# Performance work log

Measured on AMD Instinct MI355X. Metric: run time of the kernel, lower is better.

## Reference

```python
import jax, jax.numpy as jnp
import numpy as np

N, H, DDE, NH = 256, 256, 64, 4

def setup_inputs() -> dict:
    key = jax.random.key(0)
    ks = jax.random.split(key, 12)
    rn = lambda k, s, sc=1.0: (jax.random.normal(k, s) * sc).astype(jnp.float32)
    return {
        "action_hidden_state": rn(ks[0], (N, H)),
        "goal_hidden_state": rn(ks[1], (N, H)),
        "goal": rn(ks[2], (N, 2)),
        "action": rn(ks[3], (N, 2)),
        "W_dist": rn(ks[4], (8, DDE), 0.3),          # distEmbedding Linear(8, dde)
        "b_dist": jnp.zeros((DDE,), jnp.float32),
        "W_gate": rn(ks[5], (DDE, H), 0.1),          # gateFC Linear(dde, H)
        "b_gate": jnp.zeros((H,), jnp.float32),
        "w": rn(ks[6], (NH, 1, H, H), 0.06),         # GAT per-head projection
        "a": rn(ks[7], (1, 1, 2 * H, 1), 0.06),      # attention vector
        "bias": jnp.zeros((H,), jnp.float32),
    }

def reference(action_hidden_state, goal_hidden_state, goal, action,
              W_dist, b_dist, W_gate, b_gate, w, a, bias):
    n = goal.shape[0]
    # --- InteractionGate.cal_gate: x1[i,j] = x[j], x2[i,j] = x[i] ---
    g1 = jnp.broadcast_to(goal[None, :, :], (n, n, 2))
    g2 = jnp.broadcast_to(goal[:, None, :], (n, n, 2))
    a1 = jnp.broadcast_to(action[None, :, :], (n, n, 2))
    a2 = jnp.broadcast_to(action[:, None, :], (n, n, 2))
    dist = jnp.concatenate([a2, g2, a1, g1], axis=-1)                 # [n,n,8]
    gate = jax.nn.sigmoid(jax.nn.relu(dist @ W_dist + b_dist) @ W_gate + b_gate)  # [n,n,H]
    # temp_action_1[i,j] = action_hidden_state[j]
    gate_action = gate * jnp.tanh(action_hidden_state[None, :, :])    # [n,n,H]
    # diagonal entries replaced by goal_hidden_state (mask_goal = eye)
    eye = jnp.eye(n, dtype=bool)[:, :, None]
    gated_h = jnp.where(eye, goal_hidden_state[None, :, :], gate_action)  # [n,n,H]

    # --- GAT assembly: h_self[i,k] = ahs[i]; h_other = cat(ahs, gated_h) ---
    h_other = jnp.concatenate([action_hidden_state[:, None, :], gated_h], axis=1)  # [n,n+1,H]

    wm = w[:, 0]          # [NH,H,H]
    a_flat = a[0, 0, :, 0]  # [2H]
    f = wm.shape[-1]
    n_head = wm.shape[0]
    # h_self rows along k are all identical -> project once per (head, node)
    hsp = jnp.einsum('nh,zhf->znf', action_hidden_state, wm)          # [NH,n,f]
    hop = jnp.einsum('nkh,zhf->znkf', h_other, wm)                    # [NH,n,n+1,f]
    # cat([h_self', h_other']) @ a  ==  h_self'@a[:f] + h_other'@a[f:]
    score = (hsp @ a_flat[:f])[:, :, None] + hop @ a_flat[f:]         # [NH,n,n+1]
    e = jnp.where(score > 0, score, 0.2 * score)                      # LeakyReLU(0.2)
    alpha = jax.nn.softmax(e, axis=-1)                                # softmax over neighbors
    # h_attn = matmul(h_other, w) == hop; weighted sum over k, mean over heads
    out = jnp.einsum('znk,znkf->nf', alpha, hop) / n_head             # [n,f]
    return jax.nn.relu(out) + bias
```

## Files before the change

### kernel.cpp

```cpp
#include <hip/hip_runtime.h>
#include <hip/hip_bf16.h>

#define NN 256
#define HH 256

typedef __attribute__((ext_vector_type(8))) short short8;
typedef __attribute__((ext_vector_type(4))) short s16x4;
typedef __attribute__((ext_vector_type(4))) float f32x4;

__device__ __forceinline__ ushort f2bf(float x) {
    __hip_bfloat16 h = __float2bfloat16(x);
    return *reinterpret_cast<ushort*>(&h);
}
template <int CTRL>
__device__ __forceinline__ float dpp_add(float x) {
    int y = __builtin_amdgcn_update_dpp(0, __float_as_int(x), CTRL, 0xF, 0xF, true);
    return x + __int_as_float(y);
}
__device__ __forceinline__ float red16(float v) {
    v = dpp_add<0xB1>(v);
    v = dpp_add<0x4E>(v);
    v = dpp_add<0x141>(v);
    v = dpp_add<0x140>(v);
    return v;
}

#define WS_P   0
#define WS_Q   16384
#define WS_T   32768
#define WS_WA  98304
#define WS_WB  99328
#define WS_WGT 100352
#define WS_PV  104448
#define WS_ML  1153024
#define WS_VN  1161216

__global__ __launch_bounds__(256) void precompute_kernel(
    const float* __restrict__ ahs, const float* __restrict__ goal,
    const float* __restrict__ action, const float* __restrict__ Wd,
    const float* __restrict__ b_dist, const float* __restrict__ Wg,
    const float* __restrict__ w, const float* __restrict__ a,
    float* __restrict__ ws)
{
    const int b = blockIdx.x;
    const int t = threadIdx.x;
    float* P  = ws + WS_P;
    float* Q  = ws + WS_Q;
    float* T  = ws + WS_T;
    float* WA = ws + WS_WA;
    float* WB = ws + WS_WB;
    ushort* WgT = (ushort*)(ws + WS_WGT);

    if (b < NN) {
        T[b*HH + t] = tanhf(ahs[b*HH + t]);
        if (t < 64) {
            float a0 = action[2*b], a1 = action[2*b+1];
            float g0 = goal[2*b],   g1 = goal[2*b+1];
            P[b*64 + t] = a0*Wd[0*64+t] + a1*Wd[1*64+t]
                        + g0*Wd[2*64+t] + g1*Wd[3*64+t] + b_dist[t];
            Q[b*64 + t] = a0*Wd[4*64+t] + a1*Wd[5*64+t]
                        + g0*Wd[6*64+t] + g1*Wd[7*64+t];
        }
    } else if (b < NN + 16) {
        const int r    = b - NN;
        const int z    = r >> 2;
        const int rg   = r & 3;
        const int wid  = t >> 6;
        const int lane = t & 63;
        const int hbase = rg*64 + wid*16;
        const f32x4 aB = *(const f32x4*)(a + lane*4);
        const f32x4 aA = *(const f32x4*)(a + HH + lane*4);
#pragma unroll 4
        for (int rr = 0; rr < 16; ++rr) {
            const int h = hbase + rr;
            const f32x4 w4 = *(const f32x4*)(w + z*HH*HH + h*HH + lane*4);
            float dA = w4.x*aA.x + w4.y*aA.y + w4.z*aA.z + w4.w*aA.w;
            float dB = w4.x*aB.x + w4.y*aB.y + w4.z*aB.z + w4.w*aB.w;
#pragma unroll
            for (int off = 32; off; off >>= 1) {
                dA += __shfl_xor(dA, off);
                dB += __shfl_xor(dB, off);
            }
            if (lane == 0) { WA[z*HH + h] = dA; WB[z*HH + h] = dB; }
        }
    } else {
#pragma unroll 8
        for (int d = 0; d < 64; ++d) WgT[t*64 + d] = f2bf(Wg[d*HH + t]);
    }
}

__global__ __launch_bounds__(256, 4) void gat_partial_kernel(
    const float* __restrict__ ahs, const float* __restrict__ ghs,
    const float* __restrict__ b_gate, float* __restrict__ ws)
{
    const int n    = blockIdx.x & 255;
    const int qq   = blockIdx.x >> 8;
    const int t    = threadIdx.x;
    const int wid  = t >> 6;
    const int lane = t & 63;
    const int quad = lane >> 4;
    const int l15  = lane & 15;
    const int n0   = wid * 64;

    const float* P  = ws + WS_P;
    const float* Q  = ws + WS_Q;
    const float* T  = ws + WS_T;
    const float* WA = ws + WS_WA;
    const float* WB = ws + WS_WB;
    const ushort* WgT = (const ushort*)(ws + WS_WGT);
    float* PV = ws + WS_PV;
    float* ML = ws + WS_ML;

    __shared__ ushort hidb[16][72];
    __shared__ __align__(16) float part[4][16][4];
    __shared__ __align__(16) float alpha_s[16][4];
    __shared__ __align__(16) float scl4[4];
    __shared__ float m_s[4], l_s[4], cz_s[4];
    __shared__ float vred[4][4][260];

    int hcol[4];
#pragma unroll
    for (int nt = 0; nt < 4; ++nt) hcol[nt] = n0 + nt*16 + l15;

    short8 bfrag[4][2];
    float  wa_reg[4][4];
    float  bgv[4];
#pragma unroll
    for (int nt = 0; nt < 4; ++nt) {
#pragma unroll
        for (int kh = 0; kh < 2; ++kh)
            bfrag[nt][kh] = *(const short8*)(WgT + hcol[nt]*64 + kh*32 + quad*8);
#pragma unroll
        for (int z = 0; z < 4; ++z) wa_reg[z][nt] = WA[z*HH + hcol[nt]];
        bgv[nt] = b_gate[hcol[nt]];
    }

    float vacc[4][4];
    {
        float av[4];
#pragma unroll
        for (int nt = 0; nt < 4; ++nt) av[nt] = ahs[n*HH + hcol[nt]];
#pragma unroll
        for (int z = 0; z < 4; ++z)
#pragma unroll
            for (int nt = 0; nt < 4; ++nt)
                vacc[z][nt] = (qq == 0 && quad == 0) ? av[nt] : 0.f;
    }

    const int jj_own = t >> 4;
    const int db     = (t & 15) * 4;
    float pn[4];
#pragma unroll
    for (int i = 0; i < 4; ++i) pn[i] = P[n*64 + db + i];

    {
        float pc = 0.f, ps = 0.f;
        for (int h = lane; h < HH; h += 64) {
            float av = ahs[n*HH + h];
            pc = fmaf(av, WB[wid*HH + h], pc);
            ps = fmaf(av, WA[wid*HH + h], ps);
        }
#pragma unroll
        for (int off = 32; off; off >>= 1) {
            pc += __shfl_xor(pc, off);
            ps += __shfl_xor(ps, off);
        }
        if (lane == 0) {
            cz_s[wid] = pc;
            if (qq == 0) {
                float sc = pc + ps;
                float e0 = sc > 0.f ? sc : 0.2f * sc;
                m_s[wid] = e0;
                l_s[wid] = 1.0f;
            } else {
                m_s[wid] = -__builtin_inff();
                l_s[wid] = 0.0f;
            }
        }
    }
    __syncthreads();

    for (int cc = 0; cc < 4; ++cc) {
        const int j0 = qq*64 + cc*16;

        {
            const int j = j0 + jj_own;
            const float4 qa = *(const float4*)(Q + j*64 + db);
            ushort hv[4];
            hv[0] = f2bf(fmaxf(pn[0] + qa.x, 0.f));
            hv[1] = f2bf(fmaxf(pn[1] + qa.y, 0.f));
            hv[2] = f2bf(fmaxf(pn[2] + qa.z, 0.f));
            hv[3] = f2bf(fmaxf(pn[3] + qa.w, 0.f));
            *(s16x4*)&hidb[jj_own][db] = *(s16x4*)hv;
        }
        __syncthreads();

        f32x4 acc[4];
#pragma unroll
        for (int nt = 0; nt < 4; ++nt) acc[nt] = (f32x4){0.f,0.f,0.f,0.f};
        short8 afrag[2];
#pragma unroll
        for (int kh = 0; kh < 2; ++kh)
            afrag[kh] = *(const short8*)&hidb[l15][kh*32 + quad*8];
#pragma unroll
        for (int nt = 0; nt < 4; ++nt) {
            acc[nt] = __builtin_amdgcn_mfma_f32_16x16x32_bf16(
                afrag[0], bfrag[nt][0], acc[nt], 0, 0, 0);
            acc[nt] = __builtin_amdgcn_mfma_f32_16x16x32_bf16(
                afrag[1], bfrag[nt][1], acc[nt], 0, 0, 0);
        }

        float vals[4][4];
#pragma unroll
        for (int r = 0; r < 4; ++r) {
            const int jg = j0 + quad*4 + r;
            const bool diag = (jg == n);
#pragma unroll
            for (int nt = 0; nt < 4; ++nt) {
                float u = acc[nt][r] + bgv[nt];
                float val;
                if (diag) {
                    val = ghs[n*HH + hcol[nt]];
                } else {
                    float g = 1.0f / (1.0f + __expf(-u));
                    val = g * T[jg*HH + hcol[nt]];
                }
                vals[nt][r] = val;
            }
        }
#pragma unroll
        for (int z = 0; z < 4; ++z) {
            float pp[4];
#pragma unroll
            for (int r = 0; r < 4; ++r) {
                float s = 0.f;
#pragma unroll
                for (int nt = 0; nt < 4; ++nt)
                    s = fmaf(vals[nt][r], wa_reg[z][nt], s);
                pp[r] = red16(s);
            }
            if (l15 == 0) {
#pragma unroll
                for (int r = 0; r < 4; ++r)
                    part[z][quad*4 + r][wid] = pp[r];
            }
        }
        __syncthreads();

        {
            const int jj = lane & 15;
            f32x4 pr = *(const f32x4*)&part[wid][jj][0];
            const bool act = lane < 16;
            float s = cz_s[wid] + ((pr.x + pr.y) + (pr.z + pr.w));
            float e = act ? (s > 0.f ? s : 0.2f * s) : -__builtin_inff();
            float mx = e;
#pragma unroll
            for (int off = 8; off; off >>= 1) mx = fmaxf(mx, __shfl_xor(mx, off));
            float m_old = m_s[wid];
            float m_new = fmaxf(m_old, mx);
            float at = act ? __expf(e - m_new) : 0.f;
            float ss = at;
#pragma unroll
            for (int off = 8; off; off >>= 1) ss += __shfl_xor(ss, off);
            if (act) alpha_s[jj][wid] = at;
            if (lane == 0) {
                float scale = __expf(m_old - m_new);
                scl4[wid] = scale;
                l_s[wid]  = l_s[wid] * scale + ss;
                m_s[wid]  = m_new;
            }
        }
        __syncthreads();

        {
            f32x4 scv = *(const f32x4*)&scl4[0];
#pragma unroll
            for (int nt = 0; nt < 4; ++nt) {
                vacc[0][nt] *= scv.x; vacc[1][nt] *= scv.y;
                vacc[2][nt] *= scv.z; vacc[3][nt] *= scv.w;
            }
#pragma unroll
            for (int r = 0; r < 4; ++r) {
                f32x4 al = *(const f32x4*)&alpha_s[quad*4 + r][0];
#pragma unroll
                for (int nt = 0; nt < 4; ++nt) {
                    float v = vals[nt][r];
                    vacc[0][nt] = fmaf(al.x, v, vacc[0][nt]);
                    vacc[1][nt] = fmaf(al.y, v, vacc[1][nt]);
                    vacc[2][nt] = fmaf(al.z, v, vacc[2][nt]);
                    vacc[3][nt] = fmaf(al.w, v, vacc[3][nt]);
                }
            }
        }
    }

#pragma unroll
    for (int z = 0; z < 4; ++z)
#pragma unroll
        for (int nt = 0; nt < 4; ++nt)
            vred[quad][z][hcol[nt]] = vacc[z][nt];
    __syncthreads();
#pragma unroll
    for (int z = 0; z < 4; ++z) {
        float s = (vred[0][z][t] + vred[1][z][t]) + (vred[2][z][t] + vred[3][z][t]);
        PV[((qq*4 + z)*NN + n)*HH + t] = s;
    }
    if (lane == 0) {
        ML[((qq*4 + wid)*NN + n)*2 + 0] = m_s[wid];
        ML[((qq*4 + wid)*NN + n)*2 + 1] = l_s[wid];
    }
}

__global__ __launch_bounds__(256) void gat_merge_kernel(float* __restrict__ ws)
{
    const int n = blockIdx.x;
    const int t = threadIdx.x;
    const float* PV = ws + WS_PV;
    const float* ML = ws + WS_ML;
    float* VN = ws + WS_VN;

    __shared__ float sq[4][4];
    if (t < 4) {
        float m[4], l[4];
#pragma unroll
        for (int q = 0; q < 4; ++q) {
            m[q] = ML[((q*4 + t)*NN + n)*2 + 0];
            l[q] = ML[((q*4 + t)*NN + n)*2 + 1];
        }
        float mm = fmaxf(fmaxf(m[0], m[1]), fmaxf(m[2], m[3]));
        float s0 = __expf(m[0]-mm), s1 = __expf(m[1]-mm);
        float s2 = __expf(m[2]-mm), s3 = __expf(m[3]-mm);
        float inv = 1.0f / (l[0]*s0 + l[1]*s1 + l[2]*s2 + l[3]*s3);
        sq[t][0] = s0*inv; sq[t][1] = s1*inv; sq[t][2] = s2*inv; sq[t][3] = s3*inv;
    }
    __syncthreads();
#pragma unroll
    for (int z = 0; z < 4; ++z) {
        float v = 0.f;
#pragma unroll
        for (int q = 0; q < 4; ++q)
            v = fmaf(sq[z][q], PV[((q*4 + z)*NN + n)*HH + t], v);
        VN[n*1024 + z*HH + t] = v;
    }
}

__global__ __launch_bounds__(256) void gat_combine_kernel(
    const float* __restrict__ w, const float* __restrict__ bias,
    const float* __restrict__ ws, float* __restrict__ out)
{
    const int n0  = (blockIdx.x >> 2) * 2;
    const int f0  = (blockIdx.x & 3) * 64;
    const int t   = threadIdx.x;
    const int wid = t >> 6;
    const int lane= t & 63;
    const int ni  = wid & 1;
    const int ko  = wid >> 1;
    const float* VN = ws + WS_VN;

    __shared__ float accL[2][64];

    const int row = __builtin_amdgcn_readfirstlane(n0 + ni);
    const float* vrow = VN + row*1024 + ko*512;
    const float* wp   = w + (ko*512)*HH + f0 + lane;

    float a0=0.f, a1=0.f, a2=0.f, a3=0.f;
#pragma unroll 8
    for (int k = 0; k < 512; k += 4) {
        a0 = fmaf(vrow[k+0], wp[(size_t)(k+0)*HH], a0);
        a1 = fmaf(vrow[k+1], wp[(size_t)(k+1)*HH], a1);
        a2 = fmaf(vrow[k+2], wp[(size_t)(k+2)*HH], a2);
        a3 = fmaf(vrow[k+3], wp[(size_t)(k+3)*HH], a3);
    }
    float acc = (a0+a1)+(a2+a3);
    if (ko == 1) accL[ni][lane] = acc;
    __syncthreads();
    if (ko == 0) {
        float tot = acc + accL[ni][lane];
        out[(n0+ni)*HH + f0 + lane] = fmaxf(0.25f*tot, 0.f) + bias[f0+lane];
    }
}

extern "C" void kernel_launch(void* const* d_in, const int* in_sizes, int n_in,
                              void* d_out, int out_size, void* d_ws, size_t ws_size,
                              hipStream_t stream)
{
    const float* ahs    = (const float*)d_in[0];
    const float* ghs    = (const float*)d_in[1];
    const float* goal   = (const float*)d_in[2];
    const float* action = (const float*)d_in[3];
    const float* Wd     = (const float*)d_in[4];
    const float* b_dist = (const float*)d_in[5];
    const float* Wg     = (const float*)d_in[6];
    const float* b_gate = (const float*)d_in[7];
    const float* w      = (const float*)d_in[8];
    const float* a      = (const float*)d_in[9];
    const float* bias   = (const float*)d_in[10];
    float* ws   = (float*)d_ws;
    float* outp = (float*)d_out;

    precompute_kernel<<<273, 256, 0, stream>>>(ahs, goal, action, Wd, b_dist, Wg, w, a, ws);
    gat_partial_kernel<<<1024, 256, 0, stream>>>(ahs, ghs, b_gate, ws);
    gat_merge_kernel<<<256, 256, 0, stream>>>(ws);
    gat_combine_kernel<<<512, 256, 0, stream>>>(w, bias, ws, outp);
}
```

Baseline: 142.6 us.

## Use split-bf16 MFMA for output projection and cut barriers in partial kernel

The final projection now runs on MFMA tensor cores using a hi/lo bf16 split of both the merged values and the weights (three MFMAs per tile) instead of scalar FMA loops. The precompute kernel is spread over more blocks and now also emits the transposed split weights. The partial kernel builds A-fragments directly in registers instead of going through shared memory, and keeps the per-head online-softmax state in registers with DPP reductions, which removes several __syncthreads per chunk. The output kernel launches only 16 blocks, so parallelism there is low, and the split-bf16 scheme is slightly less precise than fp32.

```diff
diff --git a/kernel.cpp b/kernel.cpp
--- a/kernel.cpp
+++ b/kernel.cpp
@@ -5,7 +5,6 @@
 #define HH 256
 
 typedef __attribute__((ext_vector_type(8))) short short8;
-typedef __attribute__((ext_vector_type(4))) short s16x4;
 typedef __attribute__((ext_vector_type(4))) float f32x4;
 
 __device__ __forceinline__ ushort f2bf(float x) {
@@ -17,11 +16,19 @@
     int y = __builtin_amdgcn_update_dpp(0, __float_as_int(x), CTRL, 0xF, 0xF, true);
     return x + __int_as_float(y);
 }
+template <int CTRL>
+__device__ __forceinline__ float dpp_max(float x) {
+    int y = __builtin_amdgcn_update_dpp(0, __float_as_int(x), CTRL, 0xF, 0xF, true);
+    return fmaxf(x, __int_as_float(y));
+}
 __device__ __forceinline__ float red16(float v) {
-    v = dpp_add<0xB1>(v);
-    v = dpp_add<0x4E>(v);
-    v = dpp_add<0x141>(v);
-    v = dpp_add<0x140>(v);
+    v = dpp_add<0xB1>(v); v = dpp_add<0x4E>(v);
+    v = dpp_add<0x141>(v); v = dpp_add<0x140>(v);
+    return v;
+}
+__device__ __forceinline__ float red16max(float v) {
+    v = dpp_max<0xB1>(v); v = dpp_max<0x4E>(v);
+    v = dpp_max<0x141>(v); v = dpp_max<0x140>(v);
     return v;
 }
 
@@ -31,9 +38,12 @@
 #define WS_WA  98304
 #define WS_WB  99328
 #define WS_WGT 100352
-#define WS_PV  104448
-#define WS_ML  1153024
-#define WS_VN  1161216
+#define WS_PV  108544
+#define WS_ML  1157120
+#define WS_VNH 1165312
+#define WS_VNL 1296384
+#define WS_W2H 1427456
+#define WS_W2L 1558528
 
 __global__ __launch_bounds__(256) void precompute_kernel(
     const float* __restrict__ ahs, const float* __restrict__ goal,
@@ -49,20 +59,27 @@
     float* T  = ws + WS_T;
     float* WA = ws + WS_WA;
     float* WB = ws + WS_WB;
-    ushort* WgT = (ushort*)(ws + WS_WGT);
-
-    if (b < NN) {
-        T[b*HH + t] = tanhf(ahs[b*HH + t]);
-        if (t < 64) {
-            float a0 = action[2*b], a1 = action[2*b+1];
-            float g0 = goal[2*b],   g1 = goal[2*b+1];
-            P[b*64 + t] = a0*Wd[0*64+t] + a1*Wd[1*64+t]
-                        + g0*Wd[2*64+t] + g1*Wd[3*64+t] + b_dist[t];
-            Q[b*64 + t] = a0*Wd[4*64+t] + a1*Wd[5*64+t]
-                        + g0*Wd[6*64+t] + g1*Wd[7*64+t];
-        }
-    } else if (b < NN + 16) {
-        const int r    = b - NN;
+    ushort* WgT  = (ushort*)(ws + WS_WGT);
+    ushort* W2hi = (ushort*)(ws + WS_W2H);
+    ushort* W2lo = (ushort*)(ws + WS_W2L);
+
+    if (b < 64) {
+        const int idx = (b*256 + t)*4;
+        float4 v = *(const float4*)(ahs + idx);
+        float4 o;
+        o.x = tanhf(v.x); o.y = tanhf(v.y); o.z = tanhf(v.z); o.w = tanhf(v.w);
+        *(float4*)(T + idx) = o;
+    } else if (b < 128) {
+        const int i = (b - 64)*4 + (t >> 6);
+        const int d = t & 63;
+        float a0 = action[2*i], a1 = action[2*i+1];
+        float g0 = goal[2*i],   g1 = goal[2*i+1];
+        P[i*64 + d] = a0*Wd[0*64+d] + a1*Wd[1*64+d]
+                    + g0*Wd[2*64+d] + g1*Wd[3*64+d] + b_dist[d];
+        Q[i*64 + d] = a0*Wd[4*64+d] + a1*Wd[5*64+d]
+                    + g0*Wd[6*64+d] + g1*Wd[7*64+d];
+    } else if (b < 144) {
+        const int r    = b - 128;
         const int z    = r >> 2;
         const int rg   = r & 3;
         const int wid  = t >> 6;
@@ -83,13 +100,25 @@
             }
             if (lane == 0) { WA[z*HH + h] = dA; WB[z*HH + h] = dB; }
         }
+    } else if (b < 208) {
+        const int d = b - 144;
+        WgT[t*64 + d] = f2bf(Wg[d*HH + t]);
     } else {
-#pragma unroll 8
-        for (int d = 0; d < 64; ++d) WgT[t*64 + d] = f2bf(Wg[d*HH + t]);
-    }
-}
-
-__global__ __launch_bounds__(256, 4) void gat_partial_kernel(
+        const int kb = b - 208;
+#pragma unroll
+        for (int kk = 0; kk < 4; ++kk) {
+            const int k = kb*4 + kk;
+            float x  = w[k*HH + t];
+            ushort hi = f2bf(x);
+            __hip_bfloat16 hb = *reinterpret_cast<__hip_bfloat16*>(&hi);
+            ushort lo = f2bf(x - __bfloat162float(hb));
+            W2hi[t*1024 + k] = hi;
+            W2lo[t*1024 + k] = lo;
+        }
+    }
+}
+
+__global__ __launch_bounds__(256) void gat_partial_kernel(
     const float* __restrict__ ahs, const float* __restrict__ ghs,
     const float* __restrict__ b_gate, float* __restrict__ ws)
 {
@@ -100,6 +129,8 @@
     const int lane = t & 63;
     const int quad = lane >> 4;
     const int l15  = lane & 15;
+    const int zg   = quad;
+    const int jj   = l15;
     const int n0   = wid * 64;
 
     const float* P  = ws + WS_P;
@@ -111,11 +142,8 @@
     float* PV = ws + WS_PV;
     float* ML = ws + WS_ML;
 
-    __shared__ ushort hidb[16][72];
-    __shared__ __align__(16) float part[4][16][4];
-    __shared__ __align__(16) float alpha_s[16][4];
-    __shared__ __align__(16) float scl4[4];
-    __shared__ float m_s[4], l_s[4], cz_s[4];
+    __shared__ __align__(16) float part[2][4][16][4];
+    __shared__ __align__(16) float alpha_w[4][16][4];
     __shared__ float vred[4][4][260];
 
     int hcol[4];
@@ -135,6 +163,13 @@
         bgv[nt] = b_gate[hcol[nt]];
     }
 
+    float pnA[2][8];
+#pragma unroll
+    for (int kh = 0; kh < 2; ++kh) {
+        *(f32x4*)&pnA[kh][0] = *(const f32x4*)(P + n*64 + kh*32 + quad*8);
+        *(f32x4*)&pnA[kh][4] = *(const f32x4*)(P + n*64 + kh*32 + quad*8 + 4);
+    }
+
     float vacc[4][4];
     {
         float av[4];
@@ -147,61 +182,66 @@
                 vacc[z][nt] = (qq == 0 && quad == 0) ? av[nt] : 0.f;
     }
 
-    const int jj_own = t >> 4;
-    const int db     = (t & 15) * 4;
-    float pn[4];
-#pragma unroll
-    for (int i = 0; i < 4; ++i) pn[i] = P[n*64 + db + i];
-
+    float cz_r, m_r, l_r;
     {
         float pc = 0.f, ps = 0.f;
-        for (int h = lane; h < HH; h += 64) {
-            float av = ahs[n*HH + h];
-            pc = fmaf(av, WB[wid*HH + h], pc);
-            ps = fmaf(av, WA[wid*HH + h], ps);
-        }
-#pragma unroll
-        for (int off = 32; off; off >>= 1) {
-            pc += __shfl_xor(pc, off);
-            ps += __shfl_xor(ps, off);
-        }
-        if (lane == 0) {
-            cz_s[wid] = pc;
-            if (qq == 0) {
-                float sc = pc + ps;
-                float e0 = sc > 0.f ? sc : 0.2f * sc;
-                m_s[wid] = e0;
-                l_s[wid] = 1.0f;
-            } else {
-                m_s[wid] = -__builtin_inff();
-                l_s[wid] = 0.0f;
-            }
-        }
-    }
-    __syncthreads();
+        const int hb = jj*16;
+#pragma unroll
+        for (int i4 = 0; i4 < 4; ++i4) {
+            f32x4 av = *(const f32x4*)(ahs + n*HH + hb + i4*4);
+            f32x4 wb = *(const f32x4*)(WB + zg*HH + hb + i4*4);
+            f32x4 wa = *(const f32x4*)(WA + zg*HH + hb + i4*4);
+            pc = fmaf(av.x, wb.x, pc); pc = fmaf(av.y, wb.y, pc);
+            pc = fmaf(av.z, wb.z, pc); pc = fmaf(av.w, wb.w, pc);
+            ps = fmaf(av.x, wa.x, ps); ps = fmaf(av.y, wa.y, ps);
+            ps = fmaf(av.z, wa.z, ps); ps = fmaf(av.w, wa.w, ps);
+        }
+        pc = red16(pc); ps = red16(ps);
+        cz_r = pc;
+        if (qq == 0) {
+            float sc = pc + ps;
+            m_r = sc > 0.f ? sc : 0.2f * sc;
+            l_r = 1.0f;
+        } else {
+            m_r = -__builtin_inff();
+            l_r = 0.0f;
+        }
+    }
 
     for (int cc = 0; cc < 4; ++cc) {
-        const int j0 = qq*64 + cc*16;
-
-        {
-            const int j = j0 + jj_own;
-            const float4 qa = *(const float4*)(Q + j*64 + db);
-            ushort hv[4];
-            hv[0] = f2bf(fmaxf(pn[0] + qa.x, 0.f));
-            hv[1] = f2bf(fmaxf(pn[1] + qa.y, 0.f));
-            hv[2] = f2bf(fmaxf(pn[2] + qa.z, 0.f));
-            hv[3] = f2bf(fmaxf(pn[3] + qa.w, 0.f));
-            *(s16x4*)&hidb[jj_own][db] = *(s16x4*)hv;
-        }
-        __syncthreads();
+        const int j0  = qq*64 + cc*16;
+        const int par = cc & 1;
+
+        float tval[4][4];
+#pragma unroll
+        for (int r = 0; r < 4; ++r) {
+            const int jg = j0 + quad*4 + r;
+#pragma unroll
+            for (int nt = 0; nt < 4; ++nt)
+                tval[nt][r] = T[jg*HH + hcol[nt]];
+        }
+
+        short8 afrag[2];
+#pragma unroll
+        for (int kh = 0; kh < 2; ++kh) {
+            const float* qrow = Q + (j0 + l15)*64 + kh*32 + quad*8;
+            f32x4 qa = *(const f32x4*)qrow;
+            f32x4 qb = *(const f32x4*)(qrow + 4);
+            ushort hv[8];
+            hv[0] = f2bf(fmaxf(pnA[kh][0] + qa.x, 0.f));
+            hv[1] = f2bf(fmaxf(pnA[kh][1] + qa.y, 0.f));
+            hv[2] = f2bf(fmaxf(pnA[kh][2] + qa.z, 0.f));
+            hv[3] = f2bf(fmaxf(pnA[kh][3] + qa.w, 0.f));
+            hv[4] = f2bf(fmaxf(pnA[kh][4] + qb.x, 0.f));
+            hv[5] = f2bf(fmaxf(pnA[kh][5] + qb.y, 0.f));
+            hv[6] = f2bf(fmaxf(pnA[kh][6] + qb.z, 0.f));
+            hv[7] = f2bf(fmaxf(pnA[kh][7] + qb.w, 0.f));
+            afrag[kh] = *(short8*)hv;
+        }
 
         f32x4 acc[4];
 #pragma unroll
         for (int nt = 0; nt < 4; ++nt) acc[nt] = (f32x4){0.f,0.f,0.f,0.f};
-        short8 afrag[2];
-#pragma unroll
-        for (int kh = 0; kh < 2; ++kh)
-            afrag[kh] = *(const short8*)&hidb[l15][kh*32 + quad*8];
 #pragma unroll
         for (int nt = 0; nt < 4; ++nt) {
             acc[nt] = __builtin_amdgcn_mfma_f32_16x16x32_bf16(
@@ -223,73 +263,66 @@
                     val = ghs[n*HH + hcol[nt]];
                 } else {
                     float g = 1.0f / (1.0f + __expf(-u));
-                    val = g * T[jg*HH + hcol[nt]];
+                    val = g * tval[nt][r];
                 }
                 vals[nt][r] = val;
             }
         }
-#pragma unroll
-        for (int z = 0; z < 4; ++z) {
-            float pp[4];
+
+        float ppv[4][4];
+#pragma unroll
+        for (int z = 0; z < 4; ++z)
 #pragma unroll
             for (int r = 0; r < 4; ++r) {
                 float s = 0.f;
 #pragma unroll
                 for (int nt = 0; nt < 4; ++nt)
                     s = fmaf(vals[nt][r], wa_reg[z][nt], s);
-                pp[r] = red16(s);
+                ppv[z][r] = red16(s);
             }
-            if (l15 == 0) {
-#pragma unroll
-                for (int r = 0; r < 4; ++r)
-                    part[z][quad*4 + r][wid] = pp[r];
+        if (l15 < 4) {
+#pragma unroll
+            for (int r = 0; r < 4; ++r) {
+                float v = (l15 == 0) ? ppv[0][r] : (l15 == 1) ? ppv[1][r]
+                        : (l15 == 2) ? ppv[2][r] : ppv[3][r];
+                part[par][l15][quad*4 + r][wid] = v;
             }
         }
         __syncthreads();
 
+        float scl0, scl1, scl2, scl3;
         {
-            const int jj = lane & 15;
-            f32x4 pr = *(const f32x4*)&part[wid][jj][0];
-            const bool act = lane < 16;
-            float s = cz_s[wid] + ((pr.x + pr.y) + (pr.z + pr.w));
-            float e = act ? (s > 0.f ? s : 0.2f * s) : -__builtin_inff();
-            float mx = e;
-#pragma unroll
-            for (int off = 8; off; off >>= 1) mx = fmaxf(mx, __shfl_xor(mx, off));
-            float m_old = m_s[wid];
-            float m_new = fmaxf(m_old, mx);
-            float at = act ? __expf(e - m_new) : 0.f;
-            float ss = at;
-#pragma unroll
-            for (int off = 8; off; off >>= 1) ss += __shfl_xor(ss, off);
-            if (act) alpha_s[jj][wid] = at;
-            if (lane == 0) {
-                float scale = __expf(m_old - m_new);
-                scl4[wid] = scale;
-                l_s[wid]  = l_s[wid] * scale + ss;
-                m_s[wid]  = m_new;
-            }
-        }
-        __syncthreads();
-
-        {
-            f32x4 scv = *(const f32x4*)&scl4[0];
+            f32x4 pr = *(const f32x4*)&part[par][zg][jj][0];
+            float s = cz_r + ((pr.x + pr.y) + (pr.z + pr.w));
+            float e = s > 0.f ? s : 0.2f * s;
+            float mx = red16max(e);
+            float m_new = fmaxf(m_r, mx);
+            float at = __expf(e - m_new);
+            float ss = red16(at);
+            float scale = __expf(m_r - m_new);
+            l_r = l_r * scale + ss;
+            m_r = m_new;
+            alpha_w[wid][jj][zg] = at;
+            scl0 = __shfl(scale, 0);
+            scl1 = __shfl(scale, 16);
+            scl2 = __shfl(scale, 32);
+            scl3 = __shfl(scale, 48);
+        }
+#pragma unroll
+        for (int nt = 0; nt < 4; ++nt) {
+            vacc[0][nt] *= scl0; vacc[1][nt] *= scl1;
+            vacc[2][nt] *= scl2; vacc[3][nt] *= scl3;
+        }
+#pragma unroll
+        for (int r = 0; r < 4; ++r) {
+            f32x4 al = *(const f32x4*)&alpha_w[wid][quad*4 + r][0];
 #pragma unroll
             for (int nt = 0; nt < 4; ++nt) {
-                vacc[0][nt] *= scv.x; vacc[1][nt] *= scv.y;
-                vacc[2][nt] *= scv.z; vacc[3][nt] *= scv.w;
-            }
-#pragma unroll
-            for (int r = 0; r < 4; ++r) {
-                f32x4 al = *(const f32x4*)&alpha_s[quad*4 + r][0];
-#pragma unroll
-                for (int nt = 0; nt < 4; ++nt) {
-                    float v = vals[nt][r];
-                    vacc[0][nt] = fmaf(al.x, v, vacc[0][nt]);
-                    vacc[1][nt] = fmaf(al.y, v, vacc[1][nt]);
-                    vacc[2][nt] = fmaf(al.z, v, vacc[2][nt]);
-                    vacc[3][nt] = fmaf(al.w, v, vacc[3][nt]);
-                }
+                float v = vals[nt][r];
+                vacc[0][nt] = fmaf(al.x, v, vacc[0][nt]);
+                vacc[1][nt] = fmaf(al.y, v, vacc[1][nt]);
+                vacc[2][nt] = fmaf(al.z, v, vacc[2][nt]);
+                vacc[3][nt] = fmaf(al.w, v, vacc[3][nt]);
             }
         }
     }
@@ -305,9 +338,9 @@
         float s = (vred[0][z][t] + vred[1][z][t]) + (vred[2][z][t] + vred[3][z][t]);
         PV[((qq*4 + z)*NN + n)*HH + t] = s;
     }
-    if (lane == 0) {
-        ML[((qq*4 + wid)*NN + n)*2 + 0] = m_s[wid];
-        ML[((qq*4 + wid)*NN + n)*2 + 1] = l_s[wid];
+    if (wid == 0 && l15 == 0) {
+        ML[((qq*4 + quad)*NN + n)*2 + 0] = m_r;
+        ML[((qq*4 + quad)*NN + n)*2 + 1] = l_r;
     }
 }
 
@@ -317,7 +350,8 @@
     const int t = threadIdx.x;
     const float* PV = ws + WS_PV;
     const float* ML = ws + WS_ML;
-    float* VN = ws + WS_VN;
+    ushort* VNhi = (ushort*)(ws + WS_VNH);
+    ushort* VNlo = (ushort*)(ws + WS_VNL);
 
     __shared__ float sq[4][4];
     if (t < 4) {
@@ -340,43 +374,63 @@
 #pragma unroll
         for (int q = 0; q < 4; ++q)
             v = fmaf(sq[z][q], PV[((q*4 + z)*NN + n)*HH + t], v);
-        VN[n*1024 + z*HH + t] = v;
-    }
-}
-
-__global__ __launch_bounds__(256) void gat_combine_kernel(
-    const float* __restrict__ w, const float* __restrict__ bias,
-    const float* __restrict__ ws, float* __restrict__ out)
+        ushort hi = f2bf(v);
+        __hip_bfloat16 hb = *reinterpret_cast<__hip_bfloat16*>(&hi);
+        ushort lo = f2bf(v - __bfloat162float(hb));
+        VNhi[n*1024 + z*HH + t] = hi;
+        VNlo[n*1024 + z*HH + t] = lo;
+    }
+}
+
+__global__ __launch_bounds__(256) void gat_out_kernel(
+    const float* __restrict__ bias, const float* __restrict__ ws,
+    float* __restrict__ out)
 {
-    const int n0  = (blockIdx.x >> 2) * 2;
+    const int n0b = (blockIdx.x >> 2) * 64;
     const int f0  = (blockIdx.x & 3) * 64;
-    const int t   = threadIdx.x;
-    const int wid = t >> 6;
-    const int lane= t & 63;
-    const int ni  = wid & 1;
-    const int ko  = wid >> 1;
-    const float* VN = ws + WS_VN;
-
-    __shared__ float accL[2][64];
-
-    const int row = __builtin_amdgcn_readfirstlane(n0 + ni);
-    const float* vrow = VN + row*1024 + ko*512;
-    const float* wp   = w + (ko*512)*HH + f0 + lane;
-
-    float a0=0.f, a1=0.f, a2=0.f, a3=0.f;
-#pragma unroll 8
-    for (int k = 0; k < 512; k += 4) {
-        a0 = fmaf(vrow[k+0], wp[(size_t)(k+0)*HH], a0);
-        a1 = fmaf(vrow[k+1], wp[(size_t)(k+1)*HH], a1);
-        a2 = fmaf(vrow[k+2], wp[(size_t)(k+2)*HH], a2);
-        a3 = fmaf(vrow[k+3], wp[(size_t)(k+3)*HH], a3);
-    }
-    float acc = (a0+a1)+(a2+a3);
-    if (ko == 1) accL[ni][lane] = acc;
-    __syncthreads();
-    if (ko == 0) {
-        float tot = acc + accL[ni][lane];
-        out[(n0+ni)*HH + f0 + lane] = fmaxf(0.25f*tot, 0.f) + bias[f0+lane];
+    const int t    = threadIdx.x;
+    const int wid  = t >> 6;
+    const int lane = t & 63;
+    const int quad = lane >> 4;
+    const int l15  = lane & 15;
+    const int n0   = n0b + wid*16;
+
+    const ushort* VNhi = (const ushort*)(ws + WS_VNH);
+    const ushort* VNlo = (const ushort*)(ws + WS_VNL);
+    const ushort* W2hi = (const ushort*)(ws + WS_W2H);
+    const ushort* W2lo = (const ushort*)(ws + WS_W2L);
+
+    f32x4 acc[4];
+#pragma unroll
+    for (int nt = 0; nt < 4; ++nt) acc[nt] = (f32x4){0.f,0.f,0.f,0.f};
+
+    const ushort* arow_h = VNhi + (n0 + l15)*1024 + quad*8;
+    const ushort* arow_l = VNlo + (n0 + l15)*1024 + quad*8;
+
+    for (int ks = 0; ks < 32; ++ks) {
+        const int k0 = ks * 32;
+        short8 ah = *(const short8*)(arow_h + k0);
+        short8 al = *(const short8*)(arow_l + k0);
+#pragma unroll
+        for (int nt = 0; nt < 4; ++nt) {
+            const ushort* bbase = W2hi + (f0 + nt*16 + l15)*1024 + k0 + quad*8;
+            short8 bh = *(const short8*)bbase;
+            short8 bl = *(const short8*)(bbase + (WS_W2L - WS_W2H)*2);
+            acc[nt] = __builtin_amdgcn_mfma_f32_16x16x32_bf16(ah, bh, acc[nt], 0, 0, 0);
+            acc[nt] = __builtin_amdgcn_mfma_f32_16x16x32_bf16(ah, bl, acc[nt], 0, 0, 0);
+            acc[nt] = __builtin_amdgcn_mfma_f32_16x16x32_bf16(al, bh, acc[nt], 0, 0, 0);
+        }
+    }
+
+#pragma unroll
+    for (int nt = 0; nt < 4; ++nt) {
+        const int f = f0 + nt*16 + l15;
+        float bv = bias[f];
+#pragma unroll
+        for (int r = 0; r < 4; ++r) {
+            const int nrow = n0 + quad*4 + r;
+            out[nrow*HH + f] = fmaxf(0.25f * acc[nt][r], 0.f) + bv;
+        }
     }
 }
 
@@ -398,8 +452,8 @@
     float* ws   = (float*)d_ws;
     float* outp = (float*)d_out;
 
-    precompute_kernel<<<273, 256, 0, stream>>>(ahs, goal, action, Wd, b_dist, Wg, w, a, ws);
+    precompute_kernel<<<464, 256, 0, stream>>>(ahs, goal, action, Wd, b_dist, Wg, w, a, ws);
     gat_partial_kernel<<<1024, 256, 0, stream>>>(ahs, ghs, b_gate, ws);
     gat_merge_kernel<<<256, 256, 0, stream>>>(ws);
-    gat_combine_kernel<<<512, 256, 0, stream>>>(w, bias, ws, outp);
-}
+    gat_out_kernel<<<16, 256, 0, stream>>>(bias, ws, outp);
+}
```

Result: slower. 162.1 us (+13.7%).
